# Kernel optimization log

Hardware: AMD Instinct MI355X
Metric: run time of the kernel (lower is better)

Reference implementation:

```python
import jax, jax.numpy as jnp
import numpy as np

B, L, D = 4, 2048, 1024
E, K, FF = 8, 2, 4096
CAP_FACTOR = 1.25


def setup_inputs() -> dict:
    key = jax.random.key(0)
    ks = jax.random.split(key, 10)
    s = 0.02
    x = jax.random.normal(ks[0], (B, L, D), dtype=jnp.float32)
    noise = jax.random.normal(ks[1], (B, L, E), dtype=jnp.float32)
    Wg = jax.random.normal(ks[2], (D, E), dtype=jnp.float32) * s
    bg = jnp.zeros((E,), jnp.float32)
    Wn = jax.random.normal(ks[3], (D, E), dtype=jnp.float32) * s
    bn = jnp.zeros((E,), jnp.float32)
    W1 = jax.random.normal(ks[4], (E, D, FF), dtype=jnp.float32) * s
    b1 = jnp.zeros((E, FF), jnp.float32)
    W2 = jax.random.normal(ks[5], (E, FF, D), dtype=jnp.float32) * s
    b2 = jnp.zeros((E, D), jnp.float32)
    return {"x": x, "noise": noise, "Wg": Wg, "bg": bg, "Wn": Wn, "bn": bn,
            "W1": W1, "b1": b1, "W2": W2, "b2": b2}


def reference(x, noise, Wg, bg, Wn, bn, W1, b1, W2, b2):
    Bs, Ls, Ds = x.shape
    F_tot = Bs * Ls
    capacity = int(F_tot * K / E * CAP_FACTOR)

    # --- NoisyTopkRouter ---
    logits = jnp.einsum('bld,de->ble', x, Wg) + bg           # [B,L,E]
    noise_logits = jnp.einsum('bld,de->ble', x, Wn) + bn      # [B,L,E]
    noisy = logits + noise * jax.nn.softplus(noise_logits)
    topv, topi = jax.lax.top_k(noisy, K)                      # [B,L,K]
    # softmax over -inf-masked logits == softmax over the top-k values scattered back
    gates_k = jax.nn.softmax(topv, axis=-1)                   # [B,L,K]

    flat_x = x.reshape(F_tot, Ds)
    flat_idx = topi.reshape(F_tot, K)
    flat_gates = jnp.zeros((F_tot, E), x.dtype).at[
        jnp.arange(F_tot)[:, None], flat_idx].set(gates_k.reshape(F_tot, K))

    # --- capacity-aware dispatch (first `capacity` tokens in flat order, as torch nonzero[:capacity]) ---
    mask_EF = (flat_idx[None, :, :] == jnp.arange(E)[:, None, None]).any(-1)  # [E,F]
    pos_EF = jnp.cumsum(mask_EF, axis=1) - 1                                    # slot within expert
    keep_EF = mask_EF & (pos_EF < capacity)

    def build(keep_row, pos_row):
        buf = jnp.full((capacity,), F_tot, dtype=jnp.int32)  # sentinel -> padded zero row
        return buf.at[jnp.where(keep_row, pos_row, capacity)].set(
            jnp.arange(F_tot, dtype=jnp.int32), mode='drop')

    dispatch = jax.vmap(build)(keep_EF, pos_EF)               # [E, capacity]

    x_pad = jnp.concatenate([flat_x, jnp.zeros((1, Ds), x.dtype)], axis=0)
    g_pad = jnp.concatenate([flat_gates, jnp.zeros((1, E), x.dtype)], axis=0)

    # --- grouped expert FFN (gelu = exact, matching torch nn.GELU) ---
    xin = x_pad[dispatch]                                     # [E,C,D]
    h = jax.nn.gelu(jnp.einsum('ecd,edf->ecf', xin, W1) + b1[:, None, :], approximate=False)
    out = jnp.einsum('ecf,efd->ecd', h, W2) + b2[:, None, :]  # [E,C,D]
    gate = g_pad[dispatch, jnp.arange(E)[:, None]]            # [E,C]
    weighted = out * gate[..., None]

    # --- scatter-combine ---
    updates = jnp.zeros((F_tot + 1, Ds), x.dtype).at[dispatch.reshape(-1)].add(
        weighted.reshape(-1, Ds))
    return updates[:F_tot].reshape(Bs, Ls, Ds)
```

## Files before the change

### kernel.cpp

```cpp
#include <hip/hip_runtime.h>
#include <stdint.h>

typedef __bf16 bf16x8 __attribute__((ext_vector_type(8)));
typedef float  f32x4  __attribute__((ext_vector_type(4)));

#define F_TOT 8192
#define DIM   1024
#define NEXP  8
#define FF    4096
#define CAP   2560

__device__ __forceinline__ float b2f(unsigned short u){
    union { unsigned int u; float f; } c; c.u = ((unsigned int)u) << 16; return c.f;
}
__device__ __forceinline__ unsigned short f2b(float f){
    union { float f; unsigned int u; } c; c.f = f;
    unsigned int r = c.u + 0x7FFFu + ((c.u >> 16) & 1u);
    return (unsigned short)(r >> 16);
}
__device__ __forceinline__ float ldIn(const void* p, size_t i, int isb){
    return isb ? b2f(((const unsigned short*)p)[i]) : ((const float*)p)[i];
}
__device__ __forceinline__ void gl_lds16(const unsigned short* g, unsigned short* l){
    __builtin_amdgcn_global_load_lds(
        (const __attribute__((address_space(1))) unsigned int*)(g),
        (__attribute__((address_space(3))) unsigned int*)(l),
        16, 0, 0);
}

template<int W> __device__ __forceinline__ void waitcnt_vm(){
    if constexpr (W == 8)      asm volatile("s_waitcnt vmcnt(8)" ::: "memory");
    else if constexpr (W == 4) asm volatile("s_waitcnt vmcnt(4)" ::: "memory");
    else                       asm volatile("s_waitcnt vmcnt(0)" ::: "memory");
}

__global__ void detect_kernel(const unsigned short* __restrict__ x, int* __restrict__ flag){
    __shared__ int cnt;
    if (threadIdx.x == 0) cnt = 0;
    __syncthreads();
    unsigned short s = x[threadIdx.x];
    int e = s & 0x7F80;
    if (e >= 0x3000 && e <= 0x4800) atomicAdd(&cnt, 1);
    __syncthreads();
    if (threadIdx.x == 0) flag[0] = (cnt >= 410) ? 1 : 0;
}

__global__ void gating_kernel(const void* __restrict__ x,
                              const void* __restrict__ Wg, const void* __restrict__ bg,
                              const void* __restrict__ Wn, const void* __restrict__ bn,
                              const int* __restrict__ flag,
                              float* __restrict__ logits, float* __restrict__ nlogits)
{
    int tid = blockIdx.x * blockDim.x + threadIdx.x;
    int t = tid >> 4, o = tid & 15;
    int col = o & 7;
    int isb = flag[0];
    const void* W = (o < 8) ? Wg : Wn;
    float acc = 0.f;
    if (isb){
        const unsigned short* xr = (const unsigned short*)x + (size_t)t * DIM;
        const unsigned short* w  = (const unsigned short*)W;
        #pragma unroll 8
        for (int d = 0; d < DIM; d++) acc = fmaf(b2f(xr[d]), b2f(w[d * 8 + col]), acc);
    } else {
        const float* xr = (const float*)x + (size_t)t * DIM;
        const float* w  = (const float*)W;
        #pragma unroll 8
        for (int d = 0; d < DIM; d++) acc = fmaf(xr[d], w[d * 8 + col], acc);
    }
    acc += ldIn((o < 8) ? bg : bn, col, isb);
    ((o < 8) ? logits : nlogits)[t * 8 + col] = acc;
}

__global__ void route_kernel(const float* __restrict__ logits,
                             const float* __restrict__ nlogits,
                             const void* __restrict__ noise,
                             const int* __restrict__ flag,
                             int* __restrict__ topi, float* __restrict__ gates)
{
    int t = blockIdx.x * blockDim.x + threadIdx.x;
    int isb = flag[0];
    float ny[8];
    #pragma unroll
    for (int e = 0; e < 8; e++){
        float nl = nlogits[t * 8 + e];
        float sp = fmaxf(nl, 0.f) + log1pf(expf(-fabsf(nl)));
        ny[e] = logits[t * 8 + e] + ldIn(noise, (size_t)t * 8 + e, isb) * sp;
    }
    int i0 = 0; float v0 = ny[0];
    #pragma unroll
    for (int e = 1; e < 8; e++) if (ny[e] > v0){ v0 = ny[e]; i0 = e; }
    int i1 = -1; float v1 = -3.4e38f;
    #pragma unroll
    for (int e = 0; e < 8; e++) if (e != i0 && ny[e] > v1){ v1 = ny[e]; i1 = e; }
    float e1 = expf(v1 - v0);
    float den = 1.f + e1;
    topi[t * 2]      = i0;  topi[t * 2 + 1] = i1;
    gates[t * 2]     = 1.f / den;
    gates[t * 2 + 1] = e1 / den;
}

__global__ __launch_bounds__(1024)
void scan_kernel(const int* __restrict__ topi,
                 int* __restrict__ dispatch, int* __restrict__ slotf,
                 int* __restrict__ cntbuf)
{
    int e = blockIdx.x;
    int tid = threadIdx.x;
    for (int c = tid; c < CAP; c += 1024) dispatch[e * CAP + c] = F_TOT;
    int base = tid * 8;
    int kk[8]; int cnt = 0;
    #pragma unroll
    for (int j = 0; j < 8; j++){
        int t = base + j;
        int k = (topi[t * 2] == e) ? 0 : ((topi[t * 2 + 1] == e) ? 1 : -1);
        kk[j] = k; if (k >= 0) cnt++;
    }
    __shared__ int s[1024];
    s[tid] = cnt; __syncthreads();
    for (int off = 1; off < 1024; off <<= 1){
        int v = (tid >= off) ? s[tid - off] : 0;
        __syncthreads();
        s[tid] += v;
        __syncthreads();
    }
    if (tid == 1023) cntbuf[e] = s[1023];
    int pos = s[tid] - cnt;
    #pragma unroll
    for (int j = 0; j < 8; j++){
        if (kk[j] >= 0){
            int t = base + j;
            if (pos < CAP){
                dispatch[e * CAP + pos] = t;
                slotf[t * 2 + kk[j]] = e * CAP + pos;
            } else {
                slotf[t * 2 + kk[j]] = -1;
            }
            pos++;
        }
    }
}

__global__ void convx_kernel(const void* __restrict__ x, const int* __restrict__ flag,
                             unsigned short* __restrict__ xb)
{
    size_t i = ((size_t)blockIdx.x * blockDim.x + threadIdx.x) * 8;
    if (flag[0]){
        ushort4 a = *(const ushort4*)((const unsigned short*)x + i);
        ushort4 b = *(const ushort4*)((const unsigned short*)x + i + 4);
        *(ushort4*)(xb + i) = a;  *(ushort4*)(xb + i + 4) = b;
    } else {
        float4 a = *(const float4*)((const float*)x + i);
        float4 b = *(const float4*)((const float*)x + i + 4);
        ushort4 lo, hi;
        lo.x = f2b(a.x); lo.y = f2b(a.y); lo.z = f2b(a.z); lo.w = f2b(a.w);
        hi.x = f2b(b.x); hi.y = f2b(b.y); hi.z = f2b(b.z); hi.w = f2b(b.w);
        *(ushort4*)(xb + i) = lo; *(ushort4*)(xb + i + 4) = hi;
    }
}

__global__ void transpose_kernel(const void* __restrict__ in,
                                 unsigned short* __restrict__ out,
                                 const int* __restrict__ flag,
                                 int R, int C, int eBase)
{
    __shared__ unsigned short tile[64][68];
    const size_t mi = (size_t)(eBase + blockIdx.z) * R * C;
    const size_t mo = (size_t)blockIdx.z * R * C;
    int c0 = blockIdx.x * 64, r0 = blockIdx.y * 64;
    int t = threadIdx.x;
    int rr = t >> 4, cc = (t & 15) * 4;
    int isb = flag[0];
    #pragma unroll
    for (int i = 0; i < 4; i++){
        int r = rr + i * 16;
        size_t idx = mi + (size_t)(r0 + r) * C + c0 + cc;
        if (isb){
            ushort4 v = *(const ushort4*)((const unsigned short*)in + idx);
            *(ushort4*)&tile[r][cc] = v;
        } else {
            float4 v = *(const float4*)((const float*)in + idx);
            ushort4 u; u.x = f2b(v.x); u.y = f2b(v.y); u.z = f2b(v.z); u.w = f2b(v.w);
            *(ushort4*)&tile[r][cc] = u;
        }
    }
    __syncthreads();
    #pragma unroll
    for (int i = 0; i < 4; i++){
        int c = rr + i * 16;
        ushort4 v;
        v.x = tile[cc + 0][c]; v.y = tile[cc + 1][c];
        v.z = tile[cc + 2][c]; v.w = tile[cc + 3][c];
        *(ushort4*)(out + mo + (size_t)(c0 + c) * R + r0 + cc) = v;
    }
}


#define STAGE(k) { \
    unsigned short* sl_ = smem + (size_t)((k)&3)*(SLOT/2); \
    gl_lds16(aS0 + (size_t)(k)*32, sl_ + tid*8); \
    gl_lds16(aS1 + (size_t)(k)*32, sl_ + tid*8 + TH*8); \
    gl_lds16(bS0 + (size_t)(k)*32, sl_ + ABYTES/2 + tid*8); \
    gl_lds16(bS1 + (size_t)(k)*32, sl_ + ABYTES/2 + tid*8 + TH*8); }

#define BODY(S, DOSTAGE, VM) { \
    const int s_ = (S); \
    waitcnt_vm<VM>(); \
    __builtin_amdgcn_s_barrier(); \
    asm volatile("" ::: "memory"); \
    const char* base_ = (const char*)smem + (size_t)(s_&3)*SLOT; \
    bf16x8 afv[RM], bfv[RN]; \
    _Pragma("unroll") \
    for (int j = 0; j < RN; j++){ \
        int R_ = wn*(RN*16) + j*16 + l16; \
        bfv[j] = *(const bf16x8*)(base_ + ABYTES + (((R_<<6)|(quad<<4)) ^ sx)); \
    } \
    _Pragma("unroll") \
    for (int i = 0; i < RM; i++){ \
        int R_ = wm*(RM*16) + i*16 + l16; \
        afv[i] = *(const bf16x8*)(base_ + (((R_<<6)|(quad<<4)) ^ sx)); \
    } \
    if (DOSTAGE){ STAGE(s_+3); } \
    __builtin_amdgcn_s_setprio(1); \
    _Pragma("unroll") \
    for (int i = 0; i < RM; i++) \
        _Pragma("unroll") \
        for (int j = 0; j < RN; j++) \
            acc[i][j] = __builtin_amdgcn_mfma_f32_16x16x32_bf16(afv[i], bfv[j], acc[i][j], 0, 0, 0); \
    __builtin_amdgcn_s_setprio(0); \
}

template<int KT, int NT, int BM, int BN, int TH, int WM, int WN, bool ISF0>
__global__ __launch_bounds__(TH, 2)
void ffn_pipe_kernel(const unsigned short* __restrict__ Ain,
                     const unsigned short* __restrict__ Wt,
                     const void* __restrict__ bias,
                     const int* __restrict__ flag,
                     unsigned short* __restrict__ Out,
                     const int* __restrict__ dispatch,
                     const int* __restrict__ cnt,
                     int eBase)
{
    constexpr int NTN    = NT / BN;
    constexpr int NK     = KT / 32;
    constexpr int RM     = BM / WM / 16;
    constexpr int RN     = BN / WN / 16;
    constexpr int ABYTES = BM * 64;
    constexpr int SLOT   = (BM + BN) * 64;

    __shared__ __align__(16) unsigned short smem[SLOT * 4 / 2];

    const int el = blockIdx.y, eg = el + eBase;
    const int nt = blockIdx.x % NTN;
    const int mt = blockIdx.x / NTN;
    const int m0 = mt * BM, n0 = nt * BN;
    if (m0 >= cnt[eg]) return;

    const int tid = threadIdx.x, lane = tid & 63, wave = tid >> 6;
    const int wm = wave / WN, wn = wave % WN;
    const int quad = lane >> 4, l16 = lane & 15;
    const int sx = (l16 & 7) << 4;

    const int P0 = tid, P1 = tid + TH;
    const int LA0 = (P0 & ~7) | ((((P0>>2)^(P0>>4))&1)<<2) | ((((P0>>1)^(P0>>3))&1)<<1) | ((P0^(P0>>2)^(P0>>4))&1);
    const int LA1 = (P1 & ~7) | ((((P1>>2)^(P1>>4))&1)<<2) | ((((P1>>1)^(P1>>3))&1)<<1) | ((P1^(P1>>2)^(P1>>4))&1);
    const int rA0 = LA0 >> 2, cA0 = (LA0 & 3) * 8;
    const int rA1 = LA1 >> 2, cA1 = (LA1 & 3) * 8;

    const unsigned short *aS0, *aS1;
    if (ISF0){
        int t0 = dispatch[eg * CAP + m0 + rA0];
        int t1 = dispatch[eg * CAP + m0 + rA1];
        if (((unsigned)t0) >= (unsigned)F_TOT) t0 = 0;
        if (((unsigned)t1) >= (unsigned)F_TOT) t1 = 0;
        aS0 = Ain + (size_t)t0 * KT + cA0;
        aS1 = Ain + (size_t)t1 * KT + cA1;
    } else {
        aS0 = Ain + ((size_t)(el * CAP + m0 + rA0)) * KT + cA0;
        aS1 = Ain + ((size_t)(el * CAP + m0 + rA1)) * KT + cA1;
    }
    const unsigned short* bE  = Wt + (size_t)el * NT * KT;
    const unsigned short* bS0 = bE + (size_t)(n0 + rA0) * KT + cA0;
    const unsigned short* bS1 = bE + (size_t)(n0 + rA1) * KT + cA1;

    f32x4 acc[RM][RN] = {};

    STAGE(0); STAGE(1); STAGE(2);

    for (int s = 0; s < NK - 3; ++s){ BODY(s, 1, 8); }
    BODY(NK - 3, 0, 8);
    BODY(NK - 2, 0, 4);
    BODY(NK - 1, 0, 0);

    const int isb = flag[0];
    const int rBase = m0 + wm * (RM * 16) + quad * 4;
    const int cBase = n0 + wn * (RN * 16) + l16;
    float bv[RN];
    #pragma unroll
    for (int j = 0; j < RN; j++) bv[j] = ldIn(bias, (size_t)eg * NT + cBase + j * 16, isb);
    const int oe = ISF0 ? el : eg;
    #pragma unroll
    for (int i = 0; i < RM; i++)
        #pragma unroll
        for (int j = 0; j < RN; j++)
            #pragma unroll
            for (int r = 0; r < 4; r++){
                int row = rBase + i * 16 + r;
                float v = acc[i][j][r] + bv[j];
                if (ISF0) v = 0.5f * v * (1.0f + erff(v * 0.70710678118654752f));
                Out[((size_t)(oe * CAP + row)) * NT + cBase + j * 16] = f2b(v);
            }
}

__global__ void combine_kernel(const unsigned short* __restrict__ eo,
                               const int* __restrict__ slotf,
                               const float* __restrict__ gates,
                               const int* __restrict__ flag,
                               void* __restrict__ out)
{
    int t = blockIdx.x;
    int d = threadIdx.x * 4;
    int s0 = slotf[t * 2], s1 = slotf[t * 2 + 1];
    float g0 = gates[t * 2], g1 = gates[t * 2 + 1];
    float a0 = 0.f, a1 = 0.f, a2 = 0.f, a3 = 0.f;
    if (((unsigned)s0) < (unsigned)(NEXP * CAP)){
        ushort4 a = *(const ushort4*)(eo + (size_t)s0 * DIM + d);
        a0 += g0 * b2f(a.x); a1 += g0 * b2f(a.y);
        a2 += g0 * b2f(a.z); a3 += g0 * b2f(a.w);
    }
    if (((unsigned)s1) < (unsigned)(NEXP * CAP)){
        ushort4 a = *(const ushort4*)(eo + (size_t)s1 * DIM + d);
        a0 += g1 * b2f(a.x); a1 += g1 * b2f(a.y);
        a2 += g1 * b2f(a.z); a3 += g1 * b2f(a.w);
    }
    if (flag[0]){
        ushort4 o; o.x = f2b(a0); o.y = f2b(a1); o.z = f2b(a2); o.w = f2b(a3);
        *(ushort4*)((unsigned short*)out + (size_t)t * DIM + d) = o;
    } else {
        float4 o; o.x = a0; o.y = a1; o.z = a2; o.w = a3;
        *(float4*)((float*)out + (size_t)t * DIM + d) = o;
    }
}

extern "C" void kernel_launch(void* const* d_in, const int* in_sizes, int n_in,
                              void* d_out, int out_size, void* d_ws, size_t ws_size,
                              hipStream_t stream)
{
    const void* x     = d_in[0];
    const void* noise = d_in[1];
    const void* Wg    = d_in[2];
    const void* bg    = d_in[3];
    const void* Wn    = d_in[4];
    const void* bn    = d_in[5];
    const void* W1    = d_in[6];
    const void* b1    = d_in[7];
    const void* W2    = d_in[8];
    const void* b2    = d_in[9];
    char* ws = (char*)d_ws;

    float* logits  = (float*)(ws + 0);
    float* nlogits = (float*)(ws + 262144);
    int*   topi    = (int*)  (ws + 524288);
    float* gates   = (float*)(ws + 589824);
    int*   disp    = (int*)  (ws + 655360);
    int*   slotf   = (int*)  (ws + 737280);
    int*   flag    = (int*)  (ws + 802816);
    int*   cnt     = (int*)  (ws + 803072);
    unsigned short* xb = (unsigned short*)(ws + 1048576);
    unsigned short* Wt = (unsigned short*)(ws + 17825792);
    unsigned short* h  = (unsigned short*)(ws + 51380224);
    unsigned short* eo = (unsigned short*)(ws + 135266304);

    detect_kernel<<<1, 512, 0, stream>>>((const unsigned short*)x, flag);
    gating_kernel<<<512, 256, 0, stream>>>(x, Wg, bg, Wn, bn, flag, logits, nlogits);
    route_kernel<<<32, 256, 0, stream>>>(logits, nlogits, noise, flag, topi, gates);
    scan_kernel<<<8, 1024, 0, stream>>>(topi, disp, slotf, cnt);
    convx_kernel<<<4096, 256, 0, stream>>>(x, flag, xb);

    for (int g = 0; g < 2; g++){
        int eB = g * 4;
        transpose_kernel<<<dim3(64, 16, 4), 256, 0, stream>>>(W1, Wt, flag, DIM, FF, eB);
        ffn_pipe_kernel<DIM, FF, 256, 256, 512, 2, 4, true>
            <<<dim3((FF/256) * (CAP/256), 4), 512, 0, stream>>>(
            xb, Wt, b1, flag, h, disp, cnt, eB);
        transpose_kernel<<<dim3(16, 64, 4), 256, 0, stream>>>(W2, Wt, flag, FF, DIM, eB);
        ffn_pipe_kernel<FF, DIM, 128, 128, 256, 2, 2, false>
            <<<dim3((DIM/128) * (CAP/128), 4), 256, 0, stream>>>(
            h, Wt, b2, flag, eo, disp, cnt, eB);
    }
    combine_kernel<<<F_TOT, 256, 0, stream>>>(eo, slotf, gates, flag, d_out);
}
```

Baseline: 926.8 us.

## Double-buffer A fragments in registers to prefetch next k-step LDS reads

Splits the GEMM k-loop body into separate A-read, B-read and MFMA macros. Each iteration now loads the A fragments for the next k-step from LDS into a second register set, overlapping those LDS reads with the current MFMAs. The loop is unrolled by two to alternate the two register sets. The cost is more vector registers under the two-waves launch bound, and a tighter vmcnt wait (4 instead of 8) that leaves fewer global loads in flight.

```diff
diff --git a/kernel.cpp b/kernel.cpp
--- a/kernel.cpp
+++ b/kernel.cpp
@@ -203,32 +203,37 @@
     gl_lds16(bS0 + (size_t)(k)*32, sl_ + ABYTES/2 + tid*8); \
     gl_lds16(bS1 + (size_t)(k)*32, sl_ + ABYTES/2 + tid*8 + TH*8); }
 
-#define BODY(S, DOSTAGE, VM) { \
-    const int s_ = (S); \
-    waitcnt_vm<VM>(); \
-    __builtin_amdgcn_s_barrier(); \
-    asm volatile("" ::: "memory"); \
-    const char* base_ = (const char*)smem + (size_t)(s_&3)*SLOT; \
-    bf16x8 afv[RM], bfv[RN]; \
+#define READ_A(AF_, S_) { \
+    const char* ab_ = (const char*)smem + (size_t)((S_)&3)*SLOT; \
+    _Pragma("unroll") \
+    for (int i = 0; i < RM; i++){ \
+        int R_ = wm*(RM*16) + i*16 + l16; \
+        AF_[i] = *(const bf16x8*)(ab_ + (((R_<<6)|(quad<<4)) ^ sx)); } }
+
+#define READ_B(BF_, S_) { \
+    const char* bb_ = (const char*)smem + (size_t)((S_)&3)*SLOT + ABYTES; \
     _Pragma("unroll") \
     for (int j = 0; j < RN; j++){ \
         int R_ = wn*(RN*16) + j*16 + l16; \
-        bfv[j] = *(const bf16x8*)(base_ + ABYTES + (((R_<<6)|(quad<<4)) ^ sx)); \
-    } \
-    _Pragma("unroll") \
-    for (int i = 0; i < RM; i++){ \
-        int R_ = wm*(RM*16) + i*16 + l16; \
-        afv[i] = *(const bf16x8*)(base_ + (((R_<<6)|(quad<<4)) ^ sx)); \
-    } \
-    if (DOSTAGE){ STAGE(s_+3); } \
+        BF_[j] = *(const bf16x8*)(bb_ + (((R_<<6)|(quad<<4)) ^ sx)); } }
+
+#define MFMAS(AF_, BF_) { \
     __builtin_amdgcn_s_setprio(1); \
     _Pragma("unroll") \
     for (int i = 0; i < RM; i++) \
         _Pragma("unroll") \
         for (int j = 0; j < RN; j++) \
-            acc[i][j] = __builtin_amdgcn_mfma_f32_16x16x32_bf16(afv[i], bfv[j], acc[i][j], 0, 0, 0); \
-    __builtin_amdgcn_s_setprio(0); \
-}
+            acc[i][j] = __builtin_amdgcn_mfma_f32_16x16x32_bf16(AF_[i], BF_[j], acc[i][j], 0, 0, 0); \
+    __builtin_amdgcn_s_setprio(0); }
+
+#define ITER(S_, CUR_, NXT_, VM_, DORD_, DOST_) { \
+    waitcnt_vm<VM_>(); \
+    __builtin_amdgcn_s_barrier(); \
+    asm volatile("" ::: "memory"); \
+    READ_B(bfv, (S_)); \
+    if (DORD_){ READ_A(NXT_, (S_)+1); } \
+    if (DOST_){ STAGE((S_)+3); } \
+    MFMAS(CUR_, bfv); }
 
 template<int KT, int NT, int BM, int BN, int TH, int WM, int WN, bool ISF0>
 __global__ __launch_bounds__(TH, 2)
@@ -284,13 +289,22 @@
     const unsigned short* bS1 = bE + (size_t)(n0 + rA1) * KT + cA1;
 
     f32x4 acc[RM][RN] = {};
+    bf16x8 afA[RM], afB[RM], bfv[RN];
 
     STAGE(0); STAGE(1); STAGE(2);
-
-    for (int s = 0; s < NK - 3; ++s){ BODY(s, 1, 8); }
-    BODY(NK - 3, 0, 8);
-    BODY(NK - 2, 0, 4);
-    BODY(NK - 1, 0, 0);
+    waitcnt_vm<8>();
+    __builtin_amdgcn_s_barrier();
+    asm volatile("" ::: "memory");
+    READ_A(afA, 0);
+
+    for (int s = 0; s < NK - 4; s += 2){
+        ITER(s,     afA, afB, 4, 1, 1);
+        ITER(s + 1, afB, afA, 4, 1, 1);
+    }
+    ITER(NK - 4, afA, afB, 4, 1, 1);
+    ITER(NK - 3, afB, afA, 4, 1, 0);
+    ITER(NK - 2, afA, afB, 0, 1, 0);
+    ITER(NK - 1, afB, afA, 0, 0, 0);
 
     const int isb = flag[0];
     const int rBase = m0 + wm * (RM * 16) + quad * 4;
```

After: 916.2 us. About the same (-1.1%).
